# Kernel tuning notes

Measured on AMD Instinct MI355X. Metric: run time of the kernel, lower is better.

The kernel has to match this reference:

```python
import jax, jax.numpy as jnp
import numpy as np

N_NODES = 200000
N_EDGES = 800000
C1, E1 = 20000, 80000
C2, E2 = 2000, 8000
N_IN, N_HID, K_BLOCK = 24, 64, 6
N_OUT = 6
BN_EPS = 1e-5


def cheb_conv(x, edge_index, W, b, n):
    """PyG ChebConv with lambda_max=2: L_hat = -D^-1/2 A D^-1/2."""
    src, dst = edge_index[0], edge_index[1]
    K = W.shape[0]
    deg = jax.ops.segment_sum(jnp.ones(src.shape[0], x.dtype), dst, num_segments=n)
    dis = jnp.where(deg > 0, 1.0 / jnp.sqrt(jnp.maximum(deg, 1.0)), 0.0)
    norm = -(dis[src] * dis[dst])[:, None]  # [E,1]

    def prop(h):
        return jax.ops.segment_sum(h[src] * norm, dst, num_segments=n)

    Tx0 = x
    out = Tx0 @ W[0]
    if K > 1:
        Tx1 = prop(Tx0)
        out = out + Tx1 @ W[1]
        for k in range(2, K):
            Tx2 = 2.0 * prop(Tx1) - Tx0
            out = out + Tx2 @ W[k]
            Tx0, Tx1 = Tx1, Tx2
    return out + b


def batchnorm(h, g, bt):
    m = jnp.mean(h, axis=0)
    v = jnp.mean((h - m) ** 2, axis=0)  # biased var, as torch BN forward
    return (h - m) / jnp.sqrt(v + BN_EPS) * g + bt


def kipf_block(x, edge_index, W, b, g, bt, n):
    return jax.nn.relu(batchnorm(cheb_conv(x, edge_index, W, b, n), g, bt))


def segment_mean(x, seg, n_seg):
    s = jax.ops.segment_sum(x, seg, num_segments=n_seg)
    cnt = jax.ops.segment_sum(jnp.ones(x.shape[0], x.dtype), seg, num_segments=n_seg)
    return s / jnp.maximum(cnt, 1.0)[:, None]


def setup_inputs() -> dict:
    key = jax.random.key(0)
    ks = jax.random.split(key, 12)
    inp = {
        "x": jax.random.normal(ks[0], (N_NODES, N_IN), jnp.float32),
        "edge_index": jax.random.randint(ks[1], (2, N_EDGES), 0, N_NODES),
        "cluster1": jax.random.randint(ks[2], (N_NODES,), 0, C1),
        "cluster2": jax.random.randint(ks[3], (N_NODES,), 0, C2),
        "edge_index_c1": jax.random.randint(ks[4], (2, E1), 0, C1),
        "edge_index_c2": jax.random.randint(ks[5], (2, E2), 0, C2),
    }
    sc = 1.0 / np.sqrt(N_IN * K_BLOCK)
    for i, kk in zip((1, 2, 3), (ks[6], ks[7], ks[8])):
        inp[f"W{i}"] = jax.random.normal(kk, (K_BLOCK, N_IN, N_HID), jnp.float32) * sc
        inp[f"b{i}"] = jnp.zeros((N_HID,), jnp.float32)
        inp[f"g{i}"] = jnp.ones((N_HID,), jnp.float32)
        inp[f"bt{i}"] = jnp.zeros((N_HID,), jnp.float32)
    n_mix = 3 * N_HID + N_IN
    inp["Wm"] = jax.random.normal(ks[9], (1, n_mix, N_OUT), jnp.float32) / np.sqrt(n_mix)
    inp["bm"] = jnp.zeros((N_OUT,), jnp.float32)
    return inp


def reference(x, edge_index, cluster1, cluster2, edge_index_c1, edge_index_c2,
              W1, b1, g1, bt1, W2, b2, g2, bt2, W3, b3, g3, bt3, Wm, bm):
    # branch 1: full-resolution graph
    h1 = kipf_block(x, edge_index, W1, b1, g1, bt1, N_NODES)
    # branch 2: cluster1-pooled graph, then unpool
    xp1 = segment_mean(x, cluster1, C1)
    h2 = kipf_block(xp1, edge_index_c1, W2, b2, g2, bt2, C1)[cluster1]
    # branch 3: cluster2-pooled graph, then unpool
    xp2 = segment_mean(x, cluster2, C2)
    h3 = kipf_block(xp2, edge_index_c2, W3, b3, g3, bt3, C2)[cluster2]
    # skip concat with raw input, then mixing conv (K=1 -> identity Cheb term)
    mix = jnp.concatenate([h1, h2, h3, x], axis=1)
    return cheb_conv(mix, edge_index, Wm, bm, N_NODES)
```

## Files before the change

### kernel.cpp

```cpp
#include <hip/hip_runtime.h>
#include <algorithm>

#define FIN 24
#define NHID 64
#define NMIX 216
#define NOUT 6
#define BN_EPS 1e-5f

__global__ void k_hist(const int* __restrict__ ei, int E, int* deg) {
    int e = blockIdx.x * blockDim.x + threadIdx.x;
    if (e < E) atomicAdd(&deg[ei[E + e]], 1);
}

__global__ void k_scan_local(const int* __restrict__ deg, int n, int* rowptr, int* bsum,
                             float* __restrict__ dis) {
    __shared__ int s[256];
    int i = blockIdx.x * 256 + threadIdx.x;
    int v = (i < n) ? deg[i] : 0;
    if (i < n) dis[i] = v > 0 ? rsqrtf((float)v) : 0.f;
    s[threadIdx.x] = v;
    __syncthreads();
#pragma unroll
    for (int off = 1; off < 256; off <<= 1) {
        int x = (threadIdx.x >= off) ? s[threadIdx.x - off] : 0;
        __syncthreads();
        s[threadIdx.x] += x;
        __syncthreads();
    }
    if (i <= n) rowptr[i] = s[threadIdx.x] - v;
    if (threadIdx.x == 255) bsum[blockIdx.x] = s[255];
}

__global__ void k_scan_bsum(int* bsum, int nb) {
    __shared__ int s[256];
    int carry = 0;
    for (int base = 0; base < nb; base += 256) {
        int i = base + threadIdx.x;
        int v = (i < nb) ? bsum[i] : 0;
        s[threadIdx.x] = v;
        __syncthreads();
#pragma unroll
        for (int off = 1; off < 256; off <<= 1) {
            int x = (threadIdx.x >= off) ? s[threadIdx.x - off] : 0;
            __syncthreads();
            s[threadIdx.x] += x;
            __syncthreads();
        }
        if (i < nb) bsum[i] = s[threadIdx.x] - v + carry;
        carry += s[255];
        __syncthreads();
    }
}

__global__ void k_scan_add(int* rowptr, const int* __restrict__ bsum, int n) {
    int i = blockIdx.x * 256 + threadIdx.x;
    if (i <= n) rowptr[i] += bsum[blockIdx.x];
}

__global__ void k_fill(const int* __restrict__ ei, int E, const float* __restrict__ dis,
                       const int* __restrict__ rowptr, int* fill, int2* __restrict__ cv) {
    int e = blockIdx.x * blockDim.x + threadIdx.x;
    if (e >= E) return;
    int s = ei[e], d = ei[E + e];
    int slot = rowptr[d] + atomicAdd(&fill[d], 1);
    cv[slot] = make_int2(s, __float_as_int(-dis[s] * dis[d]));
}

__global__ void k_wt3(const float* __restrict__ Wa, float* __restrict__ Ta,
                      const float* __restrict__ Wb, float* __restrict__ Tb,
                      const float* __restrict__ Wc, float* __restrict__ Tc) {
    int o = blockIdx.x * blockDim.x + threadIdx.x;
    int which = o / 9216, oo = o - which * 9216;
    const float* W = (which == 0) ? Wa : (which == 1) ? Wb : Wc;
    float* T       = (which == 0) ? Ta : (which == 1) ? Tb : Tc;
    int k = oo / 1536, r = oo - k * 1536;
    int j = r / FIN, f = r - j * FIN;
    T[oo] = W[k * 1536 + f * NHID + j];
}

__global__ void k_propg(const int* __restrict__ rowptr, const int2* __restrict__ cv,
                        float scale, const float* __restrict__ h,
                        const float* __restrict__ prev, float* __restrict__ out, int n) {
    int idx = blockIdx.x * blockDim.x + threadIdx.x;
    if (idx >= n * 6) return;
    int d = idx / 6, q = idx - d * 6;
    int beg = rowptr[d], end = rowptr[d + 1];
    const float4* h4 = reinterpret_cast<const float4*>(h);
    float ax = 0.f, ay = 0.f, az = 0.f, aw = 0.f;
    float bx = 0.f, by = 0.f, bz = 0.f, bw = 0.f;
    int e = beg;
    for (; e + 2 <= end; e += 2) {
        int2 c0 = cv[e], c1 = cv[e + 1];
        float w0 = __int_as_float(c0.y), w1 = __int_as_float(c1.y);
        float4 h0 = h4[(size_t)c0.x * 6 + q];
        float4 h1 = h4[(size_t)c1.x * 6 + q];
        ax = fmaf(w0, h0.x, ax); ay = fmaf(w0, h0.y, ay);
        az = fmaf(w0, h0.z, az); aw = fmaf(w0, h0.w, aw);
        bx = fmaf(w1, h1.x, bx); by = fmaf(w1, h1.y, by);
        bz = fmaf(w1, h1.z, bz); bw = fmaf(w1, h1.w, bw);
    }
    if (e < end) {
        int2 c0 = cv[e];
        float w0 = __int_as_float(c0.y);
        float4 h0 = h4[(size_t)c0.x * 6 + q];
        ax = fmaf(w0, h0.x, ax); ay = fmaf(w0, h0.y, ay);
        az = fmaf(w0, h0.z, az); aw = fmaf(w0, h0.w, aw);
    }
    ax += bx; ay += by; az += bz; aw += bw;
    float4 r;
    if (prev) {
        float4 pv = reinterpret_cast<const float4*>(prev)[idx];
        r = make_float4(fmaf(scale, ax, -pv.x), fmaf(scale, ay, -pv.y),
                        fmaf(scale, az, -pv.z), fmaf(scale, aw, -pv.w));
    } else {
        r = make_float4(scale * ax, scale * ay, scale * az, scale * aw);
    }
    reinterpret_cast<float4*>(out)[idx] = r;
}

__global__ void k_gemv6(const float* __restrict__ S0, const float* __restrict__ S1,
                        const float* __restrict__ S2, const float* __restrict__ S3,
                        const float* __restrict__ S4, const float* __restrict__ S5,
                        const float* __restrict__ Wt, const float* __restrict__ bias,
                        float* __restrict__ acc, float* __restrict__ stats, int n) {
    __shared__ float sb[4][6][16 * FIN];
    int j = threadIdx.x & 63;
    int w = threadIdx.x >> 6;
    int nbase = blockIdx.x * 64 + w * 16;
#pragma unroll
    for (int k = 0; k < 9; ++k) {
        int i = k * 64 + j;
        int half = i / 96;
        int j4 = i - half * 96;
        int nd = j4 / 6, q = j4 - nd * 6;
        int node = nbase + nd;
        const float* Sh = (half == 0) ? S0 : (half == 1) ? S1 : (half == 2) ? S2
                        : (half == 3) ? S3 : (half == 4) ? S4 : S5;
        const float* src = Sh + (size_t)node * FIN + q * 4;
        float4 v = (node < n) ? *reinterpret_cast<const float4*>(src)
                              : make_float4(0.f, 0.f, 0.f, 0.f);
        *reinterpret_cast<float4*>(&sb[w][half][j4 * 4]) = v;
    }
    float accv[16];
    {
        float bb = bias[j];
#pragma unroll
        for (int nd = 0; nd < 16; ++nd) accv[nd] = bb;
    }
#pragma unroll 1
    for (int k = 0; k < 6; ++k) {
        const float4* wp = reinterpret_cast<const float4*>(Wt + k * (NHID * FIN) + j * FIN);
        float4 w0 = wp[0], w1 = wp[1], w2 = wp[2], w3 = wp[3], w4 = wp[4], w5 = wp[5];
#pragma unroll
        for (int nd = 0; nd < 16; ++nd) {
            const float4* r = reinterpret_cast<const float4*>(&sb[w][k][nd * FIN]);
            float4 v0 = r[0], v1 = r[1], v2 = r[2], v3 = r[3], v4 = r[4], v5 = r[5];
            float a = accv[nd];
            a = fmaf(v0.x, w0.x, a); a = fmaf(v0.y, w0.y, a);
            a = fmaf(v0.z, w0.z, a); a = fmaf(v0.w, w0.w, a);
            a = fmaf(v1.x, w1.x, a); a = fmaf(v1.y, w1.y, a);
            a = fmaf(v1.z, w1.z, a); a = fmaf(v1.w, w1.w, a);
            a = fmaf(v2.x, w2.x, a); a = fmaf(v2.y, w2.y, a);
            a = fmaf(v2.z, w2.z, a); a = fmaf(v2.w, w2.w, a);
            a = fmaf(v3.x, w3.x, a); a = fmaf(v3.y, w3.y, a);
            a = fmaf(v3.z, w3.z, a); a = fmaf(v3.w, w3.w, a);
            a = fmaf(v4.x, w4.x, a); a = fmaf(v4.y, w4.y, a);
            a = fmaf(v4.z, w4.z, a); a = fmaf(v4.w, w4.w, a);
            a = fmaf(v5.x, w5.x, a); a = fmaf(v5.y, w5.y, a);
            a = fmaf(v5.z, w5.z, a); a = fmaf(v5.w, w5.w, a);
            accv[nd] = a;
        }
    }
    float sum = 0.f, sq = 0.f;
#pragma unroll
    for (int nd = 0; nd < 16; ++nd) {
        int node = nbase + nd;
        if (node < n) {
            acc[(size_t)node * NHID + j] = accv[nd];
            sum += accv[nd]; sq = fmaf(accv[nd], accv[nd], sq);
        }
    }
    __shared__ float rs[256], rq[256];
    rs[threadIdx.x] = sum; rq[threadIdx.x] = sq;
    __syncthreads();
    if (threadIdx.x < 64) {
        float s = rs[threadIdx.x] + rs[threadIdx.x + 64] + rs[threadIdx.x + 128] + rs[threadIdx.x + 192];
        float q = rq[threadIdx.x] + rq[threadIdx.x + 64] + rq[threadIdx.x + 128] + rq[threadIdx.x + 192];
        atomicAdd(&stats[threadIdx.x], s);
        atomicAdd(&stats[NHID + threadIdx.x], q);
    }
}

__global__ void k_bnprep3(const float* __restrict__ st1, const float* __restrict__ g1,
                          const float* __restrict__ bt1, float inv1,
                          const float* __restrict__ st2, const float* __restrict__ g2,
                          const float* __restrict__ bt2, float inv2,
                          const float* __restrict__ st3, const float* __restrict__ g3,
                          const float* __restrict__ bt3, float inv3,
                          float* __restrict__ s1, float* __restrict__ s2,
                          float* __restrict__ s3) {
    int b = threadIdx.x >> 6, i = threadIdx.x & 63;
    const float* st = (b == 0) ? st1 : (b == 1) ? st2 : st3;
    const float* g  = (b == 0) ? g1  : (b == 1) ? g2  : g3;
    const float* bt = (b == 0) ? bt1 : (b == 1) ? bt2 : bt3;
    float inv       = (b == 0) ? inv1 : (b == 1) ? inv2 : inv3;
    float* so       = (b == 0) ? s1  : (b == 1) ? s2  : s3;
    float m = st[i] * inv;
    float v = st[NHID + i] * inv - m * m;
    float sc = g[i] * rsqrtf(v + BN_EPS);
    so[i] = sc;
    so[NHID + i] = fmaf(-m, sc, bt[i]);
}

__global__ void k_scatter(const float* __restrict__ x, const int* __restrict__ cl,
                          int n, float* xp, float* cnt) {
    int idx = blockIdx.x * blockDim.x + threadIdx.x;
    if (idx >= n * FIN) return;
    int node = idx / FIN, f = idx - node * FIN;
    int c = cl[node];
    atomicAdd(&xp[c * FIN + f], x[idx]);
    if (f == 0) atomicAdd(&cnt[c], 1.f);
}

__global__ void k_divcnt(float* xp, const float* __restrict__ cnt, int c) {
    int idx = blockIdx.x * blockDim.x + threadIdx.x;
    if (idx >= c * FIN) return;
    xp[idx] = xp[idx] / fmaxf(cnt[idx / FIN], 1.f);
}

__global__ void k_final(const float* __restrict__ acc1, const float* __restrict__ sc1,
                        const float* __restrict__ h2, const float* __restrict__ sc2,
                        const int* __restrict__ cl1,
                        const float* __restrict__ h3, const float* __restrict__ sc3,
                        const int* __restrict__ cl2,
                        const float* __restrict__ x, const float* __restrict__ Wm,
                        const float* __restrict__ bm, float* __restrict__ out, int n) {
    int t = blockIdx.x * blockDim.x + threadIdx.x;
    if (t >= n) return;
    float o[NOUT];
#pragma unroll
    for (int j = 0; j < NOUT; ++j) o[j] = bm[j];
    {
        const float4* r4 = reinterpret_cast<const float4*>(acc1 + (size_t)t * NHID);
#pragma unroll
        for (int i4 = 0; i4 < NHID / 4; ++i4) {
            float4 v = r4[i4];
            float hv[4] = {v.x, v.y, v.z, v.w};
#pragma unroll
            for (int c = 0; c < 4; ++c) {
                int i = i4 * 4 + c;
                float h = fmaxf(fmaf(hv[c], sc1[i], sc1[NHID + i]), 0.f);
#pragma unroll
                for (int j = 0; j < NOUT; ++j) o[j] = fmaf(h, Wm[i * NOUT + j], o[j]);
            }
        }
    }
    {
        const float4* r4 = reinterpret_cast<const float4*>(h2 + (size_t)cl1[t] * NHID);
#pragma unroll
        for (int i4 = 0; i4 < NHID / 4; ++i4) {
            float4 v = r4[i4];
            float hv[4] = {v.x, v.y, v.z, v.w};
#pragma unroll
            for (int c = 0; c < 4; ++c) {
                int hid = i4 * 4 + c;
                float h = fmaxf(fmaf(hv[c], sc2[hid], sc2[NHID + hid]), 0.f);
#pragma unroll
                for (int j = 0; j < NOUT; ++j) o[j] = fmaf(h, Wm[(NHID + hid) * NOUT + j], o[j]);
            }
        }
    }
    {
        const float4* r4 = reinterpret_cast<const float4*>(h3 + (size_t)cl2[t] * NHID);
#pragma unroll
        for (int i4 = 0; i4 < NHID / 4; ++i4) {
            float4 v = r4[i4];
            float hv[4] = {v.x, v.y, v.z, v.w};
#pragma unroll
            for (int c = 0; c < 4; ++c) {
                int hid = i4 * 4 + c;
                float h = fmaxf(fmaf(hv[c], sc3[hid], sc3[NHID + hid]), 0.f);
#pragma unroll
                for (int j = 0; j < NOUT; ++j) o[j] = fmaf(h, Wm[(2 * NHID + hid) * NOUT + j], o[j]);
            }
        }
    }
    {
        const float4* r4 = reinterpret_cast<const float4*>(x + (size_t)t * FIN);
#pragma unroll
        for (int i4 = 0; i4 < FIN / 4; ++i4) {
            float4 v = r4[i4];
            float hv[4] = {v.x, v.y, v.z, v.w};
#pragma unroll
            for (int c = 0; c < 4; ++c) {
                int i = 3 * NHID + i4 * 4 + c;
#pragma unroll
                for (int j = 0; j < NOUT; ++j) o[j] = fmaf(hv[c], Wm[i * NOUT + j], o[j]);
            }
        }
    }
    float* op = out + (size_t)t * NOUT;
#pragma unroll
    for (int j = 0; j < NOUT; ++j) op[j] = o[j];
}

extern "C" void kernel_launch(void* const* d_in, const int* in_sizes, int n_in,
                              void* d_out, int out_size, void* d_ws, size_t ws_size,
                              hipStream_t stream) {
    const int N = 200000, E = 800000;
    const int C1n = 20000, E1 = 80000;
    const int C2n = 2000, E2 = 8000;

    const float* x  = (const float*)d_in[0];
    const int* ei   = (const int*)d_in[1];
    const int* cl1  = (const int*)d_in[2];
    const int* cl2  = (const int*)d_in[3];
    const int* eic1 = (const int*)d_in[4];
    const int* eic2 = (const int*)d_in[5];
    const float* W1 = (const float*)d_in[6];  const float* b1 = (const float*)d_in[7];
    const float* g1 = (const float*)d_in[8];  const float* bt1 = (const float*)d_in[9];
    const float* W2 = (const float*)d_in[10]; const float* b2 = (const float*)d_in[11];
    const float* g2 = (const float*)d_in[12]; const float* bt2 = (const float*)d_in[13];
    const float* W3 = (const float*)d_in[14]; const float* b3 = (const float*)d_in[15];
    const float* g3 = (const float*)d_in[16]; const float* bt3 = (const float*)d_in[17];
    const float* Wm = (const float*)d_in[18]; const float* bm = (const float*)d_in[19];

    char* wb = (char*)d_ws;
    size_t off = 0;
    auto alloc = [&](size_t nwords) {
        void* p = wb + off; off += ((nwords + 3) & ~(size_t)3) * 4; return p;
    };
    int* degi1 = (int*)alloc(N);   int* fill1 = (int*)alloc(N);
    int* degi2 = (int*)alloc(C1n); int* fill2 = (int*)alloc(C1n);
    int* degi3 = (int*)alloc(C2n); int* fill3 = (int*)alloc(C2n);
    float* st1 = (float*)alloc(128); float* st2 = (float*)alloc(128); float* st3 = (float*)alloc(128);
    float* xp1 = (float*)alloc((size_t)C1n * FIN); float* cnt1 = (float*)alloc(C1n);
    float* xp2 = (float*)alloc((size_t)C2n * FIN); float* cnt2 = (float*)alloc(C2n);
    size_t zero_bytes = off;
    int* rp1 = (int*)alloc(N + 1);   int2* cv1 = (int2*)alloc(2 * (size_t)E);
    int* rp2 = (int*)alloc(C1n + 1); int2* cv2 = (int2*)alloc(2 * (size_t)E1);
    int* rp3 = (int*)alloc(C2n + 1); int2* cv3 = (int2*)alloc(2 * (size_t)E2);
    float* dis1 = (float*)alloc(N); float* dis2 = (float*)alloc(C1n); float* dis3 = (float*)alloc(C2n);
    int* bsum = (int*)alloc(1024);
    float* scsh1 = (float*)alloc(128); float* scsh2 = (float*)alloc(128); float* scsh3 = (float*)alloc(128);
    float* Wt1 = (float*)alloc(9216); float* Wt2 = (float*)alloc(9216); float* Wt3 = (float*)alloc(9216);
    float* T1[5]; for (int i = 0; i < 5; ++i) T1[i] = (float*)alloc((size_t)N * FIN);
    float* T2[5]; for (int i = 0; i < 5; ++i) T2[i] = (float*)alloc((size_t)C1n * FIN);
    float* T3[5]; for (int i = 0; i < 5; ++i) T3[i] = (float*)alloc((size_t)C2n * FIN);
    float* acc1 = (float*)alloc((size_t)N * NHID);
    float* acc2 = (float*)alloc((size_t)C1n * NHID);
    float* acc3 = (float*)alloc((size_t)C2n * NHID);
    if (off > ws_size) return;

    hipMemsetAsync(d_ws, 0, zero_bytes, stream);

    const int T = 256;
    auto cdiv = [](int a, int b) { return (a + b - 1) / b; };

    k_wt3<<<cdiv(3 * 9216, T), T, 0, stream>>>(W1, Wt1, W2, Wt2, W3, Wt3);

    auto branch = [&](const float* xin, int n, const int* e, int Ecnt,
                      const float* Wt, const float* bb, int* degi, int* fill, float* dis,
                      int* rp, int2* cv, float** Tb, float* acc, float* st) {
        int ge = cdiv(Ecnt, T);
        int nb = cdiv(n + 1, 256);
        int gg = cdiv(n, 64);
        int gp = cdiv(n * 6, T);
        k_hist<<<ge, T, 0, stream>>>(e, Ecnt, degi);
        k_scan_local<<<nb, 256, 0, stream>>>(degi, n, rp, bsum, dis);
        k_scan_bsum<<<1, 256, 0, stream>>>(bsum, nb);
        k_scan_add<<<nb, 256, 0, stream>>>(rp, bsum, n);
        k_fill<<<ge, T, 0, stream>>>(e, Ecnt, dis, rp, fill, cv);
        k_propg<<<gp, T, 0, stream>>>(rp, cv, 1.0f, xin, nullptr, Tb[0], n);
        k_propg<<<gp, T, 0, stream>>>(rp, cv, 2.0f, Tb[0], xin, Tb[1], n);
        k_propg<<<gp, T, 0, stream>>>(rp, cv, 2.0f, Tb[1], Tb[0], Tb[2], n);
        k_propg<<<gp, T, 0, stream>>>(rp, cv, 2.0f, Tb[2], Tb[1], Tb[3], n);
        k_propg<<<gp, T, 0, stream>>>(rp, cv, 2.0f, Tb[3], Tb[2], Tb[4], n);
        k_gemv6<<<gg, T, 0, stream>>>(xin, Tb[0], Tb[1], Tb[2], Tb[3], Tb[4],
                                      Wt, bb, acc, st, n);
    };

    branch(x, N, ei, E, Wt1, b1, degi1, fill1, dis1, rp1, cv1, T1, acc1, st1);
    k_scatter<<<cdiv(N * FIN, T), T, 0, stream>>>(x, cl1, N, xp1, cnt1);
    k_divcnt<<<cdiv(C1n * FIN, T), T, 0, stream>>>(xp1, cnt1, C1n);
    branch(xp1, C1n, eic1, E1, Wt2, b2, degi2, fill2, dis2, rp2, cv2, T2, acc2, st2);
    k_scatter<<<cdiv(N * FIN, T), T, 0, stream>>>(x, cl2, N, xp2, cnt2);
    k_divcnt<<<cdiv(C2n * FIN, T), T, 0, stream>>>(xp2, cnt2, C2n);
    branch(xp2, C2n, eic2, E2, Wt3, b3, degi3, fill3, dis3, rp3, cv3, T3, acc3, st3);
    k_bnprep3<<<1, 192, 0, stream>>>(st1, g1, bt1, 1.0f / (float)N,
                                     st2, g2, bt2, 1.0f / (float)C1n,
                                     st3, g3, bt3, 1.0f / (float)C2n,
                                     scsh1, scsh2, scsh3);
    k_final<<<cdiv(N, T), T, 0, stream>>>(acc1, scsh1, acc2, scsh2, cl1,
                                          acc3, scsh3, cl2,
                                          x, Wm, bm, (float*)d_out, N);
}
```

Before: 658.9 us.

## Unroll propagation gather, drop LDS staging in gemv, fuse cluster scatters

The sparse propagation loop now handles four edges per iteration with independent accumulators, so more gathers are in flight at once. The gemv kernel drops its shared-memory staging and reads node features directly from global memory with a wave-uniform base, relying on cache broadcast. The two cluster-pooling scatter kernels are merged into one pass over x, which halves the reads of x. Reading directly from global memory in the gemv may increase load traffic or latency compared with the LDS staging it replaces.

Result: no change. 666.1 us (+1.1%).

```diff
diff --git a/kernel.cpp b/kernel.cpp
--- a/kernel.cpp
+++ b/kernel.cpp
@@ -88,7 +88,26 @@
     const float4* h4 = reinterpret_cast<const float4*>(h);
     float ax = 0.f, ay = 0.f, az = 0.f, aw = 0.f;
     float bx = 0.f, by = 0.f, bz = 0.f, bw = 0.f;
+    float cx = 0.f, cy = 0.f, cz = 0.f, cw = 0.f;
+    float dx = 0.f, dy = 0.f, dz = 0.f, dw = 0.f;
     int e = beg;
+    for (; e + 4 <= end; e += 4) {
+        int2 c0 = cv[e], c1 = cv[e + 1], c2 = cv[e + 2], c3 = cv[e + 3];
+        float w0 = __int_as_float(c0.y), w1 = __int_as_float(c1.y);
+        float w2 = __int_as_float(c2.y), w3 = __int_as_float(c3.y);
+        float4 h0 = h4[(size_t)c0.x * 6 + q];
+        float4 h1 = h4[(size_t)c1.x * 6 + q];
+        float4 h2 = h4[(size_t)c2.x * 6 + q];
+        float4 h3 = h4[(size_t)c3.x * 6 + q];
+        ax = fmaf(w0, h0.x, ax); ay = fmaf(w0, h0.y, ay);
+        az = fmaf(w0, h0.z, az); aw = fmaf(w0, h0.w, aw);
+        bx = fmaf(w1, h1.x, bx); by = fmaf(w1, h1.y, by);
+        bz = fmaf(w1, h1.z, bz); bw = fmaf(w1, h1.w, bw);
+        cx = fmaf(w2, h2.x, cx); cy = fmaf(w2, h2.y, cy);
+        cz = fmaf(w2, h2.z, cz); cw = fmaf(w2, h2.w, cw);
+        dx = fmaf(w3, h3.x, dx); dy = fmaf(w3, h3.y, dy);
+        dz = fmaf(w3, h3.z, dz); dw = fmaf(w3, h3.w, dw);
+    }
     for (; e + 2 <= end; e += 2) {
         int2 c0 = cv[e], c1 = cv[e + 1];
         float w0 = __int_as_float(c0.y), w1 = __int_as_float(c1.y);
@@ -106,7 +125,8 @@
         ax = fmaf(w0, h0.x, ax); ay = fmaf(w0, h0.y, ay);
         az = fmaf(w0, h0.z, az); aw = fmaf(w0, h0.w, aw);
     }
-    ax += bx; ay += by; az += bz; aw += bw;
+    ax += bx + cx + dx; ay += by + cy + dy;
+    az += bz + cz + dz; aw += bw + cw + dw;
     float4 r;
     if (prev) {
         float4 pv = reinterpret_cast<const float4*>(prev)[idx];
@@ -123,24 +143,9 @@
                         const float* __restrict__ S4, const float* __restrict__ S5,
                         const float* __restrict__ Wt, const float* __restrict__ bias,
                         float* __restrict__ acc, float* __restrict__ stats, int n) {
-    __shared__ float sb[4][6][16 * FIN];
     int j = threadIdx.x & 63;
     int w = threadIdx.x >> 6;
-    int nbase = blockIdx.x * 64 + w * 16;
-#pragma unroll
-    for (int k = 0; k < 9; ++k) {
-        int i = k * 64 + j;
-        int half = i / 96;
-        int j4 = i - half * 96;
-        int nd = j4 / 6, q = j4 - nd * 6;
-        int node = nbase + nd;
-        const float* Sh = (half == 0) ? S0 : (half == 1) ? S1 : (half == 2) ? S2
-                        : (half == 3) ? S3 : (half == 4) ? S4 : S5;
-        const float* src = Sh + (size_t)node * FIN + q * 4;
-        float4 v = (node < n) ? *reinterpret_cast<const float4*>(src)
-                              : make_float4(0.f, 0.f, 0.f, 0.f);
-        *reinterpret_cast<float4*>(&sb[w][half][j4 * 4]) = v;
-    }
+    int nbase = __builtin_amdgcn_readfirstlane(blockIdx.x * 64 + (w << 4));
     float accv[16];
     {
         float bb = bias[j];
@@ -149,11 +154,15 @@
     }
 #pragma unroll 1
     for (int k = 0; k < 6; ++k) {
+        const float* Sk = (k == 0) ? S0 : (k == 1) ? S1 : (k == 2) ? S2
+                        : (k == 3) ? S3 : (k == 4) ? S4 : S5;
         const float4* wp = reinterpret_cast<const float4*>(Wt + k * (NHID * FIN) + j * FIN);
         float4 w0 = wp[0], w1 = wp[1], w2 = wp[2], w3 = wp[3], w4 = wp[4], w5 = wp[5];
 #pragma unroll
         for (int nd = 0; nd < 16; ++nd) {
-            const float4* r = reinterpret_cast<const float4*>(&sb[w][k][nd * FIN]);
+            int node = nbase + nd;
+            int nodec = (node < n) ? node : (n - 1);
+            const float4* r = reinterpret_cast<const float4*>(Sk + (size_t)nodec * FIN);
             float4 v0 = r[0], v1 = r[1], v2 = r[2], v3 = r[3], v4 = r[4], v5 = r[5];
             float a = accv[nd];
             a = fmaf(v0.x, w0.x, a); a = fmaf(v0.y, w0.y, a);
@@ -212,14 +221,17 @@
     so[NHID + i] = fmaf(-m, sc, bt[i]);
 }
 
-__global__ void k_scatter(const float* __restrict__ x, const int* __restrict__ cl,
-                          int n, float* xp, float* cnt) {
+__global__ void k_scatter2(const float* __restrict__ x, const int* __restrict__ cl1,
+                           const int* __restrict__ cl2, int n,
+                           float* xp1, float* cnt1, float* xp2, float* cnt2) {
     int idx = blockIdx.x * blockDim.x + threadIdx.x;
     if (idx >= n * FIN) return;
     int node = idx / FIN, f = idx - node * FIN;
-    int c = cl[node];
-    atomicAdd(&xp[c * FIN + f], x[idx]);
-    if (f == 0) atomicAdd(&cnt[c], 1.f);
+    float v = x[idx];
+    int c1 = cl1[node], c2 = cl2[node];
+    atomicAdd(&xp1[c1 * FIN + f], v);
+    atomicAdd(&xp2[c2 * FIN + f], v);
+    if (f == 0) { atomicAdd(&cnt1[c1], 1.f); atomicAdd(&cnt2[c2], 1.f); }
 }
 
 __global__ void k_divcnt(float* xp, const float* __restrict__ cnt, int c) {
@@ -381,10 +393,9 @@
     };
 
     branch(x, N, ei, E, Wt1, b1, degi1, fill1, dis1, rp1, cv1, T1, acc1, st1);
-    k_scatter<<<cdiv(N * FIN, T), T, 0, stream>>>(x, cl1, N, xp1, cnt1);
+    k_scatter2<<<cdiv(N * FIN, T), T, 0, stream>>>(x, cl1, cl2, N, xp1, cnt1, xp2, cnt2);
     k_divcnt<<<cdiv(C1n * FIN, T), T, 0, stream>>>(xp1, cnt1, C1n);
     branch(xp1, C1n, eic1, E1, Wt2, b2, degi2, fill2, dis2, rp2, cv2, T2, acc2, st2);
-    k_scatter<<<cdiv(N * FIN, T), T, 0, stream>>>(x, cl2, N, xp2, cnt2);
     k_divcnt<<<cdiv(C2n * FIN, T), T, 0, stream>>>(xp2, cnt2, C2n);
     branch(xp2, C2n, eic2, E2, Wt3, b3, degi3, fill3, dis3, rp3, cv3, T3, acc3, st3);
     k_bnprep3<<<1, 192, 0, stream>>>(st1, g1, bt1, 1.0f / (float)N,
```
